# Optimization experiments

Measured on AMD Instinct MI355X. Metric: run time of the kernel, lower is better.

## Reference

```python
import jax, jax.numpy as jnp
import numpy as np

# Mamba2 defaults with d_model=512, headdim=2*d_model (=> nheads=1)
D_MODEL = 512
D_INNER = 2 * D_MODEL          # expand=2
D_STATE = 128
NHEADS = 1                     # d_inner // headdim = 1
HEADDIM = D_INNER              # headdim = 2*hidden_dim
D_CONV = 4
NG = 1                         # ngroups
EPS = 1e-5


def setup_inputs() -> dict:
    key = jax.random.key(0)
    ks = jax.random.split(key, 8)
    B, L = 4, 2048
    d_in_proj = 2 * D_INNER + 2 * NG * D_STATE + NHEADS   # 2305
    conv_ch = D_INNER + 2 * NG * D_STATE                  # 1280
    x = jax.random.normal(ks[0], (B, L, D_MODEL), jnp.float32)
    rnn_state = jax.random.normal(ks[1], (B, D_MODEL), jnp.float32)
    W_in = jax.random.normal(ks[2], (d_in_proj, D_MODEL), jnp.float32) * (D_MODEL ** -0.5)
    conv_w = jax.random.normal(ks[3], (conv_ch, 1, D_CONV), jnp.float32) * (D_CONV ** -0.5)
    conv_b = jnp.zeros((conv_ch,), jnp.float32)
    # dt_bias = inv_softplus(dt) with dt ~ U(1e-3, 0.1), as in Mamba2 init
    dt = jax.random.uniform(ks[4], (NHEADS,), jnp.float32, 1e-3, 0.1)
    dt_bias = jnp.log(jnp.expm1(dt))
    A_log = jnp.log(jax.random.uniform(ks[5], (NHEADS,), jnp.float32, 1.0, 16.0))
    Dp = jnp.ones((NHEADS,), jnp.float32)
    norm_w = jnp.ones((D_INNER,), jnp.float32)
    W_out = jax.random.normal(ks[6], (D_MODEL, D_INNER), jnp.float32) * (D_INNER ** -0.5)
    return dict(x=x, rnn_state=rnn_state, W_in=W_in, conv_w=conv_w, conv_b=conv_b,
                dt_bias=dt_bias, A_log=A_log, Dp=Dp, norm_w=norm_w, W_out=W_out)


def _mamba2(x, W_in, conv_w, conv_b, dt_bias, A_log, Dp, norm_w, W_out):
    B, L, _ = x.shape
    zxbcdt = jnp.einsum('bld,ed->ble', x, W_in)           # (B,L,2305)
    z, xBC, dt = jnp.split(zxbcdt, [D_INNER, 2 * D_INNER + 2 * NG * D_STATE], axis=-1)
    # causal depthwise conv1d over channels (B,C,L), then silu
    xBC = xBC.transpose(0, 2, 1)
    xBC = jax.lax.conv_general_dilated(
        xBC, conv_w, window_strides=(1,), padding=[(D_CONV - 1, 0)],
        feature_group_count=xBC.shape[1], dimension_numbers=('NCH', 'OIH', 'NCH'))
    xBC = jax.nn.silu(xBC + conv_b[None, :, None]).transpose(0, 2, 1)
    xs, Bm, Cm = jnp.split(xBC, [D_INNER, D_INNER + NG * D_STATE], axis=-1)
    xs = xs.reshape(B, L, NHEADS, HEADDIM)
    dt = jax.nn.softplus(dt + dt_bias)                    # (B,L,H)
    A = -jnp.exp(A_log)                                   # (H,)
    dA = jnp.exp(dt * A)                                  # (B,L,H)

    # selective state-space scan: h_t = dA_t*h_{t-1} + dt_t * x_t (x) B_t ; y_t = h_t @ C_t
    def step(state, inp):
        x_t, dt_t, dA_t, B_t, C_t = inp
        state = dA_t[:, :, None, None] * state \
            + (dt_t[:, :, None] * x_t)[..., None] * B_t[:, None, None, :]
        y_t = jnp.einsum('bhpn,bn->bhp', state, C_t)
        return state, y_t

    init = jnp.zeros((B, NHEADS, HEADDIM, D_STATE), x.dtype)
    inputs = (xs.transpose(1, 0, 2, 3), dt.transpose(1, 0, 2), dA.transpose(1, 0, 2),
              Bm.transpose(1, 0, 2), Cm.transpose(1, 0, 2))
    _, ys = jax.lax.scan(step, init, inputs)              # (L,B,H,P)
    y = ys.transpose(1, 0, 2, 3) + Dp[None, None, :, None] * xs
    y = y.reshape(B, L, D_INNER)
    # gated RMSNorm (gate first, norm_before_gate=False)
    y = y * jax.nn.silu(z)
    y = y * jax.lax.rsqrt(jnp.mean(y * y, axis=-1, keepdims=True) + EPS) * norm_w
    return jnp.einsum('bld,od->blo', y, W_out)


def reference(x, rnn_state, W_in, conv_w, conv_b, dt_bias, A_log, Dp, norm_w, W_out):
    out = _mamba2(x, W_in, conv_w, conv_b, dt_bias, A_log, Dp, norm_w, W_out)
    return (out, rnn_state)
```

## Files before the change

kernel.cpp:

```cpp
#include <hip/hip_runtime.h>
#include <cstdint>
#include <cstddef>


typedef __bf16 bf16_t;
typedef __bf16 bf16x8 __attribute__((ext_vector_type(8)));
typedef __bf16 bf16x4 __attribute__((ext_vector_type(4)));
typedef __bf16 bf16x2 __attribute__((ext_vector_type(2)));
typedef float  f32x4  __attribute__((ext_vector_type(4)));

#define BATCH   4
#define SEQLEN  2048
#define MROWS   8192
#define DMODEL  512
#define DINNER  1024
#define DSTATE  128
#define NZX     2304
#define NCONV   1280
#define CHUNK   128
#define NCHUNK  16
#define NBC     64

__device__ __forceinline__ float siluf(float x) { return x / (1.f + __expf(-x)); }

__device__ __forceinline__ void load_lds16(const bf16_t* g, bf16_t* l)
{
    __builtin_amdgcn_global_load_lds(
        (const __attribute__((address_space(1))) void*)g,
        (__attribute__((address_space(3))) void*)l,
        16, 0, 0);
}

template <typename OutT>
__device__ __forceinline__ void gemm64_body(
    unsigned char* smem,
    const bf16_t* __restrict__ A, const bf16_t* __restrict__ B,
    OutT* __restrict__ C, int Ntot, int K, int lda, int ldb, int bn, int bm)
{
    bf16_t* As = (bf16_t*)smem;
    bf16_t* Bs = (bf16_t*)(smem + 8192);

    const int tid  = threadIdx.x;
    const int wave = tid >> 6, lane = tid & 63;
    const int lr = lane & 15, q = lane >> 4;
    const int wm = (wave & 1) * 32, wn = (wave >> 1) * 64;

    f32x4 acc[2][4];
    #pragma unroll
    for (int i = 0; i < 2; ++i)
        #pragma unroll
        for (int j = 0; j < 4; ++j)
            acc[i][j] = (f32x4){0.f, 0.f, 0.f, 0.f};

    const int row_a0 = bm * 64, row_b0 = bn * 128;
    const int srow = tid >> 3;
    const int gsw  = (((tid & 7) ^ (srow & 7))) * 8;
    const int lsl  = (tid & 7) * 8;

    for (int kt = 0; kt < K; kt += 64) {
        #pragma unroll
        for (int i = 0; i < 2; ++i) {
            int row = srow + i * 32;
            load_lds16(&A[(size_t)(row_a0 + row) * lda + kt + gsw], &As[row * 64 + lsl]);
        }
        #pragma unroll
        for (int i = 0; i < 4; ++i) {
            int row = srow + i * 32;
            load_lds16(&B[(size_t)(row_b0 + row) * ldb + kt + gsw], &Bs[row * 64 + lsl]);
        }
        __syncthreads();
        #pragma unroll
        for (int k0 = 0; k0 < 64; k0 += 32) {
            bf16x8 af[2], bfr[4];
            #pragma unroll
            for (int mi = 0; mi < 2; ++mi) {
                int r = wm + mi * 16 + lr, kc = (k0 >> 3) + q;
                af[mi] = *reinterpret_cast<const bf16x8*>(
                    &As[r * 64 + ((kc ^ (r & 7)) << 3)]);
            }
            #pragma unroll
            for (int ni = 0; ni < 4; ++ni) {
                int r = wn + ni * 16 + lr, kc = (k0 >> 3) + q;
                bfr[ni] = *reinterpret_cast<const bf16x8*>(
                    &Bs[r * 64 + ((kc ^ (r & 7)) << 3)]);
            }
            #pragma unroll
            for (int mi = 0; mi < 2; ++mi)
                #pragma unroll
                for (int ni = 0; ni < 4; ++ni)
                    acc[mi][ni] = __builtin_amdgcn_mfma_f32_16x16x32_bf16(
                        af[mi], bfr[ni], acc[mi][ni], 0, 0, 0);
        }
        __syncthreads();
    }

    #pragma unroll
    for (int mi = 0; mi < 2; ++mi)
        #pragma unroll
        for (int ni = 0; ni < 4; ++ni)
            #pragma unroll
            for (int ri = 0; ri < 4; ++ri) {
                int row = row_a0 + wm + mi * 16 + q * 4 + ri;
                int col = row_b0 + wn + ni * 16 + lr;
                C[(size_t)row * Ntot + col] = (OutT)acc[mi][ni][ri];
            }
}

template <typename OutT>
__device__ __forceinline__ void gemm6464_body(
    unsigned char* smem,
    const bf16_t* __restrict__ A, const bf16_t* __restrict__ B,
    OutT* __restrict__ C, int Ntot, int K, int lda, int ldb, int bn, int bm)
{
    bf16_t* As = (bf16_t*)smem;
    bf16_t* Bs = (bf16_t*)(smem + 8192);

    const int tid  = threadIdx.x;
    const int wave = tid >> 6, lane = tid & 63;
    const int lr = lane & 15, q = lane >> 4;
    const int wm = (wave & 1) * 32, wn = (wave >> 1) * 32;

    f32x4 acc[2][2];
    #pragma unroll
    for (int i = 0; i < 2; ++i)
        #pragma unroll
        for (int j = 0; j < 2; ++j)
            acc[i][j] = (f32x4){0.f, 0.f, 0.f, 0.f};

    const int row_a0 = bm * 64, row_b0 = bn * 64;
    const int srow = tid >> 3;
    const int gsw  = (((tid & 7) ^ (srow & 7))) * 8;
    const int lsl  = (tid & 7) * 8;

    for (int kt = 0; kt < K; kt += 64) {
        #pragma unroll
        for (int i = 0; i < 2; ++i) {
            int row = srow + i * 32;
            load_lds16(&A[(size_t)(row_a0 + row) * lda + kt + gsw], &As[row * 64 + lsl]);
            load_lds16(&B[(size_t)(row_b0 + row) * ldb + kt + gsw], &Bs[row * 64 + lsl]);
        }
        __syncthreads();
        #pragma unroll
        for (int k0 = 0; k0 < 64; k0 += 32) {
            bf16x8 af[2], bfr[2];
            #pragma unroll
            for (int mi = 0; mi < 2; ++mi) {
                int r = wm + mi * 16 + lr, kc = (k0 >> 3) + q;
                af[mi] = *reinterpret_cast<const bf16x8*>(
                    &As[r * 64 + ((kc ^ (r & 7)) << 3)]);
            }
            #pragma unroll
            for (int ni = 0; ni < 2; ++ni) {
                int r = wn + ni * 16 + lr, kc = (k0 >> 3) + q;
                bfr[ni] = *reinterpret_cast<const bf16x8*>(
                    &Bs[r * 64 + ((kc ^ (r & 7)) << 3)]);
            }
            #pragma unroll
            for (int mi = 0; mi < 2; ++mi)
                #pragma unroll
                for (int ni = 0; ni < 2; ++ni)
                    acc[mi][ni] = __builtin_amdgcn_mfma_f32_16x16x32_bf16(
                        af[mi], bfr[ni], acc[mi][ni], 0, 0, 0);
        }
        __syncthreads();
    }

    #pragma unroll
    for (int mi = 0; mi < 2; ++mi)
        #pragma unroll
        for (int ni = 0; ni < 2; ++ni)
            #pragma unroll
            for (int ri = 0; ri < 4; ++ri) {
                int row = row_a0 + wm + mi * 16 + q * 4 + ri;
                int col = row_b0 + wn + ni * 16 + lr;
                C[(size_t)row * Ntot + col] = (OutT)acc[mi][ni][ri];
            }
}

__device__ __forceinline__ void cumsum_body(
    const float* __restrict__ dtv, const float* __restrict__ A_log,
    float* __restrict__ sarr, float* __restrict__ Pv,
    float* __restrict__ EdTv, float* __restrict__ chp, int bc)
{
    __shared__ float w0sum, stot;
    int j = threadIdx.x;
    bool active = j < CHUNK;
    int lane = j & 63;
    int r = bc * CHUNK + j;
    float A = -expf(A_log[0]);
    float dt = active ? dtv[r] : 0.f;
    float s = dt;
    #pragma unroll
    for (int m = 1; m <= 32; m <<= 1) {
        float o = __shfl_up(s, m);
        if (lane >= m) s += o;
    }
    if (j == 63) w0sum = s;
    __syncthreads();
    if (j >= 64 && active) s += w0sum;
    if (j == 127) stot = s;
    __syncthreads();
    if (active) {
        float sT = stot;
        sarr[r] = s;
        Pv[r]   = expf(A * s);
        EdTv[r] = expf(A * (sT - s)) * dt;
        if (j == 127) chp[bc] = expf(A * sT);
    }
}

__global__ __launch_bounds__(256) void gemm1_kernel(
    const bf16_t* __restrict__ xb, const bf16_t* __restrict__ winb,
    bf16_t* __restrict__ zx, const float* __restrict__ dtv,
    const float* __restrict__ A_log, float* __restrict__ sarr,
    float* __restrict__ Pv, float* __restrict__ EdTv, float* __restrict__ chp)
{
    __shared__ __align__(16) unsigned char smem[24576];
    int linear = blockIdx.x;
    if (linear < (NZX / 128) * (MROWS / 64)) {
        int xcd = linear & 7, j = linear >> 3;
        int bm = xcd * 16 + (j & 15);
        int bn = j >> 4;
        gemm64_body<bf16_t>(smem, xb, winb, zx, NZX, DMODEL, DMODEL, DMODEL, bn, bm);
    } else {
        cumsum_body(dtv, A_log, sarr, Pv, EdTv, chp, linear - 2304);
    }
}

__global__ __launch_bounds__(256) void gemm2_kernel(
    const bf16_t* __restrict__ yb, const bf16_t* __restrict__ woutb,
    float* __restrict__ out)
{
    __shared__ __align__(16) unsigned char smem[16384];
    int id  = blockIdx.x;
    int xcd = id & 7, j = id >> 3;
    int bm  = xcd * 16 + (j & 15);
    int bn  = j >> 4;
    gemm6464_body<float>(smem, yb, woutb, out, DMODEL, DINNER, DINNER, DINNER, bn, bm);
}

__global__ __launch_bounds__(256) void gemmA_kernel(
    const bf16_t* __restrict__ Xt, const bf16_t* __restrict__ Bwt,
    bf16_t* __restrict__ cstate)
{
    __shared__ __align__(16) unsigned char smem[16384];
    int id = blockIdx.x;
    int bc = id & 63;
    int t  = id >> 6;
    int bm = t >> 1, bn = t & 1;
    gemm6464_body<bf16_t>(smem,
        Xt + (size_t)bc * 131072, Bwt + (size_t)bc * 16384,
        cstate + (size_t)bc * 131072,
        DSTATE, CHUNK, CHUNK, CHUNK, bn, bm);
}

__device__ __forceinline__ void mbuild64_body(
    unsigned char* smem,
    const float* __restrict__ sarr, const float* __restrict__ dtv,
    const float* __restrict__ Pv, const float* __restrict__ A_log,
    const bf16_t* __restrict__ xbc, bf16_t* __restrict__ Mx, int sub)
{
    int bc = sub & 63;
    int t  = sub >> 6;
    int bm = t >> 1, bn = t & 1;

    bf16_t* Cs  = (bf16_t*)smem;
    bf16_t* Bs2 = (bf16_t*)(smem + 16384);
    float* sj = (float*)(smem + 32768);
    float* dj = sj + 128;
    float* pj = dj + 128;

    int tid = threadIdx.x;
    if (tid < CHUNK) {
        sj[tid] = sarr[bc * CHUNK + tid];
        dj[tid] = dtv[bc * CHUNK + tid];
        pj[tid] = Pv[bc * CHUNK + tid];
    }
    int rowbase = bc * 128;
    int srow = tid >> 4;
    int gsw  = (((tid & 15) ^ (srow & 7))) * 8;
    int lsl  = (tid & 15) * 8;
    #pragma unroll
    for (int i = 0; i < 4; ++i) {
        int row = srow + i * 16;
        load_lds16(&xbc[(size_t)(rowbase + bm * 64 + row) * NCONV + 1152 + gsw],
                   &Cs[row * 128 + lsl]);
        load_lds16(&xbc[(size_t)(rowbase + bn * 64 + row) * NCONV + 1024 + gsw],
                   &Bs2[row * 128 + lsl]);
    }
    __syncthreads();

    const int wave = tid >> 6, lane = tid & 63;
    const int lr = lane & 15, q = lane >> 4;
    const int wm = (wave & 1) * 32, wn = (wave >> 1) * 32;

    f32x4 acc[2][2];
    #pragma unroll
    for (int i = 0; i < 2; ++i)
        #pragma unroll
        for (int j = 0; j < 2; ++j)
            acc[i][j] = (f32x4){0.f, 0.f, 0.f, 0.f};

    #pragma unroll
    for (int k0 = 0; k0 < 128; k0 += 32) {
        bf16x8 af[2], bfr[2];
        #pragma unroll
        for (int mi = 0; mi < 2; ++mi) {
            int r = wm + mi * 16 + lr, kc = (k0 >> 3) + q;
            af[mi] = *reinterpret_cast<const bf16x8*>(
                &Cs[r * 128 + ((kc ^ (r & 7)) << 3)]);
        }
        #pragma unroll
        for (int ni = 0; ni < 2; ++ni) {
            int r = wn + ni * 16 + lr, kc = (k0 >> 3) + q;
            bfr[ni] = *reinterpret_cast<const bf16x8*>(
                &Bs2[r * 128 + ((kc ^ (r & 7)) << 3)]);
        }
        #pragma unroll
        for (int mi = 0; mi < 2; ++mi)
            #pragma unroll
            for (int ni = 0; ni < 2; ++ni)
                acc[mi][ni] = __builtin_amdgcn_mfma_f32_16x16x32_bf16(
                    af[mi], bfr[ni], acc[mi][ni], 0, 0, 0);
    }

    float A = -expf(A_log[0]);
    bf16_t* MxB = Mx + (size_t)bc * 32768;
    #pragma unroll
    for (int mi = 0; mi < 2; ++mi)
        #pragma unroll
        for (int ni = 0; ni < 2; ++ni)
            #pragma unroll
            for (int ri = 0; ri < 4; ++ri) {
                int row = bm * 64 + wm + mi * 16 + q * 4 + ri;
                int col = bn * 64 + wn + ni * 16 + lr;
                float val = 0.f;
                if (col <= row)
                    val = acc[mi][ni][ri] * expf(A * (sj[row] - sj[col])) * dj[col];
                MxB[(size_t)row * 256 + col] = (bf16_t)val;
            }

    if (bn == 0) {
        int rl = tid >> 2;
        int cb2 = (tid & 3) * 32;
        float Pi = pj[bm * 64 + rl];
        #pragma unroll
        for (int m0 = 0; m0 < 32; m0 += 8) {
            int kc = (cb2 + m0) >> 3;
            bf16x8 cv = *reinterpret_cast<const bf16x8*>(
                &Cs[rl * 128 + ((kc ^ (rl & 7)) << 3)]);
            bf16x8 o;
            #pragma unroll
            for (int m = 0; m < 8; ++m) o[m] = (bf16_t)((float)cv[m] * Pi);
            *reinterpret_cast<bf16x8*>(
                &MxB[(size_t)(bm * 64 + rl) * 256 + 128 + cb2 + m0]) = o;
        }
    }
}

__device__ __forceinline__ void scan_body(
    unsigned char* smem,
    const bf16_t* __restrict__ cstate, const float* __restrict__ chp,
    bf16_t* __restrict__ Stb, int blk)
{
    float* chS = (float*)smem;
    int idx = blk * 256 + threadIdx.x;
    int b   = idx >> 17;
    int np  = idx & 131071;
    if (threadIdx.x < NCHUNK) chS[threadIdx.x] = chp[b * NCHUNK + threadIdx.x];
    __syncthreads();

    const bf16_t* src = cstate + ((size_t)b << 21) + np;
    bf16_t*       dst = Stb    + ((size_t)b << 21) + np;
    float t[NCHUNK];
    #pragma unroll
    for (int c = 0; c < NCHUNK; ++c) t[c] = (float)src[(size_t)c << 17];
    float v = 0.f;
    #pragma unroll
    for (int c = 0; c < NCHUNK; ++c) {
        dst[(size_t)c << 17] = (bf16_t)v;
        v = chS[c] * v + t[c];
    }
}

__global__ __launch_bounds__(256) void scan_mbuild_kernel(
    const bf16_t* __restrict__ cstate, const float* __restrict__ chp,
    bf16_t* __restrict__ Stb,
    const float* __restrict__ sarr, const float* __restrict__ dtv,
    const float* __restrict__ Pv, const float* __restrict__ A_log,
    const bf16_t* __restrict__ xbc, bf16_t* __restrict__ Mx)
{
    __shared__ __align__(16) unsigned char smem[34304];
    int id = blockIdx.x;
    if (id < 256) {
        mbuild64_body(smem, sarr, dtv, Pv, A_log, xbc, Mx, id);
    } else {
        scan_body(smem, cstate, chp, Stb, id - 256);
    }
}

__global__ __launch_bounds__(256) void gemm_y_kernel(
    const bf16_t* __restrict__ Mx, const bf16_t* __restrict__ Xt,
    const bf16_t* __restrict__ Stb, bf16_t* __restrict__ yf)
{
    __shared__ __align__(16) bf16_t As[64 * 64];
    __shared__ __align__(16) bf16_t Bs[64 * 64];

    int id = blockIdx.x;
    int bc = id & 63;
    int t  = id >> 6;
    int half = t & 1, bn = t >> 1;

    const bf16_t* Ab = Mx  + (size_t)bc * 32768 + (size_t)half * 64 * 256;
    const bf16_t* Xb = Xt  + (size_t)bc * 131072 + (size_t)bn * 64 * 128;
    const bf16_t* Sb = Stb + (size_t)bc * 131072 + (size_t)bn * 64 * 128;
    bf16_t* Cb = yf + (size_t)bc * 131072 + (size_t)half * 64 * 1024;

    const int tid  = threadIdx.x;
    const int wave = tid >> 6, lane = tid & 63;
    const int lr = lane & 15, q = lane >> 4;
    const int wm = (wave & 1) * 32, wn = (wave >> 1) * 32;

    f32x4 acc[2][2];
    #pragma unroll
    for (int i = 0; i < 2; ++i)
        #pragma unroll
        for (int j = 0; j < 2; ++j)
            acc[i][j] = (f32x4){0.f, 0.f, 0.f, 0.f};

    const int srow = tid >> 3;
    const int gsw  = (((tid & 7) ^ (srow & 7))) * 8;
    const int lsl  = (tid & 7) * 8;

    for (int kt = 0; kt < 256; kt += 64) {
        const bf16_t* bsrc = (kt < 128) ? (Xb + kt) : (Sb + (kt - 128));
        #pragma unroll
        for (int i = 0; i < 2; ++i) {
            int row = srow + i * 32;
            load_lds16(&Ab[(size_t)row * 256 + kt + gsw], &As[row * 64 + lsl]);
            load_lds16(&bsrc[(size_t)row * 128 + gsw], &Bs[row * 64 + lsl]);
        }
        __syncthreads();
        #pragma unroll
        for (int k0 = 0; k0 < 64; k0 += 32) {
            bf16x8 af[2], bfr[2];
            #pragma unroll
            for (int mi = 0; mi < 2; ++mi) {
                int r = wm + mi * 16 + lr, kc = (k0 >> 3) + q;
                af[mi] = *reinterpret_cast<const bf16x8*>(
                    &As[r * 64 + ((kc ^ (r & 7)) << 3)]);
            }
            #pragma unroll
            for (int ni = 0; ni < 2; ++ni) {
                int r = wn + ni * 16 + lr, kc = (k0 >> 3) + q;
                bfr[ni] = *reinterpret_cast<const bf16x8*>(
                    &Bs[r * 64 + ((kc ^ (r & 7)) << 3)]);
            }
            #pragma unroll
            for (int mi = 0; mi < 2; ++mi)
                #pragma unroll
                for (int ni = 0; ni < 2; ++ni)
                    acc[mi][ni] = __builtin_amdgcn_mfma_f32_16x16x32_bf16(
                        af[mi], bfr[ni], acc[mi][ni], 0, 0, 0);
        }
        __syncthreads();
    }

    #pragma unroll
    for (int mi = 0; mi < 2; ++mi)
        #pragma unroll
        for (int ni = 0; ni < 2; ++ni)
            #pragma unroll
            for (int ri = 0; ri < 4; ++ri) {
                int row = wm + mi * 16 + q * 4 + ri;
                int col = bn * 64 + wn + ni * 16 + lr;
                Cb[(size_t)row * 1024 + col] = (bf16_t)acc[mi][ni][ri];
            }
}

__global__ __launch_bounds__(256) void dtcast_kernel(
    const float* __restrict__ x, const float* __restrict__ W_in,
    const float* __restrict__ dt_bias, const float* __restrict__ W_out,
    float* __restrict__ dtv, bf16_t* __restrict__ xb,
    bf16_t* __restrict__ winb, bf16_t* __restrict__ woutb)
{
    int bid = blockIdx.x;
    if (bid < MROWS / 4) {
        int wave = threadIdx.x >> 6, lane = threadIdx.x & 63;
        int r = bid * 4 + wave;
        const float* xr = x + (size_t)r * DMODEL + lane * 8;
        const float* wr = W_in + (size_t)NZX * DMODEL + lane * 8;
        float4 a0 = *reinterpret_cast<const float4*>(xr);
        float4 a1 = *reinterpret_cast<const float4*>(xr + 4);
        float4 b0 = *reinterpret_cast<const float4*>(wr);
        float4 b1 = *reinterpret_cast<const float4*>(wr + 4);

        bf16x8 xo;
        xo[0] = (bf16_t)a0.x; xo[1] = (bf16_t)a0.y; xo[2] = (bf16_t)a0.z; xo[3] = (bf16_t)a0.w;
        xo[4] = (bf16_t)a1.x; xo[5] = (bf16_t)a1.y; xo[6] = (bf16_t)a1.z; xo[7] = (bf16_t)a1.w;
        *reinterpret_cast<bf16x8*>(xb + (size_t)r * DMODEL + lane * 8) = xo;

        float s = a0.x * b0.x + a0.y * b0.y + a0.z * b0.z + a0.w * b0.w
                + a1.x * b1.x + a1.y * b1.y + a1.z * b1.z + a1.w * b1.w;
        #pragma unroll
        for (int m = 32; m >= 1; m >>= 1) s += __shfl_xor(s, m);
        if (lane == 0) {
            float t  = s + dt_bias[0];
            dtv[r] = (t > 20.f) ? t : log1pf(expf(t));
        }
        return;
    }
    int i = (bid - MROWS / 4) * 256 + threadIdx.x;
    const int n4a = 2305 * DMODEL / 4, n4b = DMODEL * DINNER / 4;
    const float* src; bf16_t* dst; int j;
    if (i < n4a)            { src = W_in;  dst = winb;  j = i; }
    else if (i < n4a + n4b) { src = W_out; dst = woutb; j = i - n4a; }
    else return;
    float4 v = reinterpret_cast<const float4*>(src)[j];
    bf16x4 o;
    o[0] = (bf16_t)v.x; o[1] = (bf16_t)v.y; o[2] = (bf16_t)v.z; o[3] = (bf16_t)v.w;
    reinterpret_cast<bf16x4*>(dst)[j] = o;
}

__global__ __launch_bounds__(256) void conv_tr_kernel(
    const bf16_t* __restrict__ zx, const float* __restrict__ cw,
    const float* __restrict__ cb, const float* __restrict__ EdTv,
    bf16_t* __restrict__ xbc, bf16_t* __restrict__ Xt, bf16_t* __restrict__ Bwt)
{
    constexpr int TS = 66;
    __shared__ bf16_t tile[128 * TS];
    __shared__ float cwS[64 * 4];
    __shared__ float cbS[64];

    int id  = blockIdx.x;
    int xcd = id & 7;
    int k   = id >> 3;
    int bc  = xcd * 8 + (k & 7);
    int rest = k >> 3;
    int cg   = rest >> 1;
    int half = rest & 1;
    int c0   = cg * 128 + half * 64;
    int tid  = threadIdx.x;

    if (tid < 64) {
        float4 w = *reinterpret_cast<const float4*>(cw + (size_t)(c0 + tid) * 4);
        *reinterpret_cast<float4*>(&cwS[tid * 4]) = w;
        cbS[tid] = cb[c0 + tid];
    }
    __syncthreads();

    int lrow = tid >> 3;
    int lc8  = (tid & 7) * 8;
    int g0 = bc * 128;

    #pragma unroll
    for (int pass = 0; pass < 4; ++pass) {
        int row = pass * 32 + lrow;
        int g = g0 + row;
        int l = g & (SEQLEN - 1);
        float acc[8];
        #pragma unroll
        for (int m = 0; m < 8; ++m) acc[m] = cbS[lc8 + m];
        #pragma unroll
        for (int kk = 0; kk < 4; ++kk) {
            if (l + kk >= 3) {
                bf16x8 v = *reinterpret_cast<const bf16x8*>(
                    zx + (size_t)(g + kk - 3) * NZX + DINNER + c0 + lc8);
                #pragma unroll
                for (int m = 0; m < 8; ++m)
                    acc[m] += cwS[(lc8 + m) * 4 + kk] * (float)v[m];
            }
        }
        bf16x8 o;
        #pragma unroll
        for (int m = 0; m < 8; ++m) o[m] = (bf16_t)siluf(acc[m]);
        *reinterpret_cast<bf16x8*>(xbc + (size_t)g * NCONV + c0 + lc8) = o;
        if (cg < 9) {
            #pragma unroll
            for (int jj = 0; jj < 4; ++jj) {
                bf16x2 p; p[0] = o[jj * 2]; p[1] = o[jj * 2 + 1];
                *reinterpret_cast<bf16x2*>(&tile[row * TS + lc8 + jj * 2]) = p;
            }
        }
    }
    if (cg == 9) return;
    __syncthreads();

    const bool isB = (cg == 8);
    int jo = (tid >> 4) * 8;
    int i  = tid & 15;
    float sc[8];
    #pragma unroll
    for (int m = 0; m < 8; ++m)
        sc[m] = isB ? EdTv[bc * 128 + jo + m] : 1.f;

    #pragma unroll
    for (int pass = 0; pass < 4; ++pass) {
        int oc = pass * 16 + i;
        bf16x8 o;
        #pragma unroll
        for (int m = 0; m < 8; ++m)
            o[m] = (bf16_t)((float)tile[(jo + m) * TS + oc] * sc[m]);
        bf16_t* dst = isB
            ? (Bwt + (size_t)bc * 16384 + (size_t)(c0 - 1024 + oc) * 128 + jo)
            : (Xt + (size_t)bc * 131072 + (size_t)(c0 + oc) * 128 + jo);
        *reinterpret_cast<bf16x8*>(dst) = o;
    }
}

__global__ __launch_bounds__(256) void gate_norm_kernel(
    const bf16_t* __restrict__ yf, const bf16_t* __restrict__ zx,
    const bf16_t* __restrict__ xbc, const float* __restrict__ Dp,
    const float* __restrict__ norm_w, bf16_t* __restrict__ yb,
    const float* __restrict__ rnn, float* __restrict__ outTail)
{
    int blk = blockIdx.x, tid = threadIdx.x;
    if (blk >= MROWS / 4) {
        int i = (blk - MROWS / 4) * 256 + tid;
        if (i < BATCH * DMODEL) outTail[i] = rnn[i];
        return;
    }
    int wave = tid >> 6, lane = tid & 63;
    int r = blk * 4 + wave;
    int p0 = lane * 8, p1 = 512 + lane * 8;
    float D0 = Dp[0];

    bf16x8 y0 = *reinterpret_cast<const bf16x8*>(yf + (size_t)r * DINNER + p0);
    bf16x8 y1 = *reinterpret_cast<const bf16x8*>(yf + (size_t)r * DINNER + p1);
    bf16x8 z0 = *reinterpret_cast<const bf16x8*>(zx + (size_t)r * NZX + p0);
    bf16x8 z1 = *reinterpret_cast<const bf16x8*>(zx + (size_t)r * NZX + p1);
    bf16x8 x0 = *reinterpret_cast<const bf16x8*>(xbc + (size_t)r * NCONV + p0);
    bf16x8 x1 = *reinterpret_cast<const bf16x8*>(xbc + (size_t)r * NCONV + p1);

    float g[16];
    #pragma unroll
    for (int m = 0; m < 8; ++m) {
        g[m]     = ((float)y0[m] + D0 * (float)x0[m]) * siluf((float)z0[m]);
        g[8 + m] = ((float)y1[m] + D0 * (float)x1[m]) * siluf((float)z1[m]);
    }
    float ss = 0.f;
    #pragma unroll
    for (int m = 0; m < 16; ++m) ss += g[m] * g[m];
    #pragma unroll
    for (int m = 32; m >= 1; m >>= 1) ss += __shfl_xor(ss, m);
    float scale = rsqrtf(ss * (1.f / 1024.f) + 1e-5f);

    const float* nw = norm_w;
    float4 w0a = *reinterpret_cast<const float4*>(nw + p0);
    float4 w0b = *reinterpret_cast<const float4*>(nw + p0 + 4);
    float4 w1a = *reinterpret_cast<const float4*>(nw + p1);
    float4 w1b = *reinterpret_cast<const float4*>(nw + p1 + 4);
    float w[16] = {w0a.x, w0a.y, w0a.z, w0a.w, w0b.x, w0b.y, w0b.z, w0b.w,
                   w1a.x, w1a.y, w1a.z, w1a.w, w1b.x, w1b.y, w1b.z, w1b.w};
    bf16x8 o0, o1;
    #pragma unroll
    for (int m = 0; m < 8; ++m) {
        o0[m] = (bf16_t)(g[m] * scale * w[m]);
        o1[m] = (bf16_t)(g[8 + m] * scale * w[8 + m]);
    }
    *reinterpret_cast<bf16x8*>(yb + (size_t)r * DINNER + p0) = o0;
    *reinterpret_cast<bf16x8*>(yb + (size_t)r * DINNER + p1) = o1;
}

extern "C" void kernel_launch(void* const* d_in, const int* in_sizes, int n_in,
                              void* d_out, int out_size, void* d_ws, size_t ws_size,
                              hipStream_t stream)
{
    const float* x        = (const float*)d_in[0];
    const float* rnn      = (const float*)d_in[1];
    const float* W_in     = (const float*)d_in[2];
    const float* conv_w   = (const float*)d_in[3];
    const float* conv_b   = (const float*)d_in[4];
    const float* dt_bias  = (const float*)d_in[5];
    const float* A_log    = (const float*)d_in[6];
    const float* Dp       = (const float*)d_in[7];
    const float* norm_w   = (const float*)d_in[8];
    const float* W_out    = (const float*)d_in[9];
    float* out = (float*)d_out;

    char* ws = (char*)d_ws;
    bf16_t* xb     = (bf16_t*)(ws + 0);
    bf16_t* Mx     = (bf16_t*)(ws + 4194304);
    bf16_t* winb   = (bf16_t*)(ws + 8388608);
    bf16_t* woutb  = (bf16_t*)(ws + 10748928);
    bf16_t* zx     = (bf16_t*)(ws + 11797504);
    float*  dtv    = (float*) (ws + 49546240);
    float*  sarr   = (float*) (ws + 49579008);
    float*  Pv     = (float*) (ws + 49611776);
    float*  EdTv   = (float*) (ws + 49644544);
    float*  chp    = (float*) (ws + 49677312);
    bf16_t* xbcb   = (bf16_t*)(ws + 49677568);
    bf16_t* Xt     = (bf16_t*)(ws + 70649088);
    bf16_t* Bwt    = (bf16_t*)(ws + 87426304);
    bf16_t* cstate = (bf16_t*)(ws + 89523456);
    bf16_t* yf     = (bf16_t*)(ws + 89523456);
    bf16_t* Stb    = (bf16_t*)(ws + 106300672);
    bf16_t* yb     = (bf16_t*)(ws + 123077888);

    {
        const int n4a = 2305 * DMODEL / 4, n4b = DMODEL * DINNER / 4;
        int grid = MROWS / 4 + (n4a + n4b + 255) / 256;
        dtcast_kernel<<<grid, 256, 0, stream>>>(
            x, W_in, dt_bias, W_out, dtv, xb, winb, woutb);
    }

    gemm1_kernel<<<2304 + NBC, 256, 0, stream>>>(
        xb, winb, zx, dtv, A_log, sarr, Pv, EdTv, chp);

    conv_tr_kernel<<<1280, 256, 0, stream>>>(
        zx, conv_w, conv_b, EdTv, xbcb, Xt, Bwt);

    gemmA_kernel<<<2048, 256, 0, stream>>>(Xt, Bwt, cstate);

    scan_mbuild_kernel<<<256 + BATCH * 131072 / 256, 256, 0, stream>>>(
        cstate, chp, Stb, sarr, dtv, Pv, A_log, xbcb, Mx);

    gemm_y_kernel<<<2048, 256, 0, stream>>>(Mx, Xt, Stb, yf);

    gate_norm_kernel<<<MROWS / 4 + 8, 256, 0, stream>>>(
        yf, zx, xbcb, Dp, norm_w, yb, rnn, out + (size_t)MROWS * DMODEL);

    gemm2_kernel<<<1024, 256, 0, stream>>>(yb, woutb, out);
}
```

Before: 190.2 us.

## Fuse gating and RMSNorm into gemm_y epilogue and gemm2 row scaling

Removes the separate gate_norm kernel. gemm_y now applies the D skip and SiLU gate in its epilogue, writes the gated y in bf16, and accumulates per-row sum of squares with atomics into a buffer that the scan kernel zeroes. gemm2 applies the rsqrt row scale to its output, and norm_w is folded into W_out during the bf16 cast. This saves one launch plus a full read and write of the intermediate y, at the cost of atomics and an epilogue that stages results through LDS.

```diff
diff --git a/kernel.cpp b/kernel.cpp
--- a/kernel.cpp
+++ b/kernel.cpp
@@ -229,14 +229,85 @@
 
 __global__ __launch_bounds__(256) void gemm2_kernel(
     const bf16_t* __restrict__ yb, const bf16_t* __restrict__ woutb,
-    float* __restrict__ out)
-{
-    __shared__ __align__(16) unsigned char smem[16384];
+    const float* __restrict__ ss, float* __restrict__ out)
+{
+    __shared__ __align__(16) bf16_t As[64 * 64];
+    __shared__ __align__(16) bf16_t Bs[64 * 64];
+
     int id  = blockIdx.x;
     int xcd = id & 7, j = id >> 3;
     int bm  = xcd * 16 + (j & 15);
     int bn  = j >> 4;
-    gemm6464_body<float>(smem, yb, woutb, out, DMODEL, DINNER, DINNER, DINNER, bn, bm);
+
+    const int tid  = threadIdx.x;
+    const int wave = tid >> 6, lane = tid & 63;
+    const int lr = lane & 15, q = lane >> 4;
+    const int wm = (wave & 1) * 32, wn = (wave >> 1) * 32;
+
+    f32x4 acc[2][2];
+    #pragma unroll
+    for (int i = 0; i < 2; ++i)
+        #pragma unroll
+        for (int jj = 0; jj < 2; ++jj)
+            acc[i][jj] = (f32x4){0.f, 0.f, 0.f, 0.f};
+
+    const int row_a0 = bm * 64, row_b0 = bn * 64;
+    const int srow = tid >> 3;
+    const int gsw  = (((tid & 7) ^ (srow & 7))) * 8;
+    const int lsl  = (tid & 7) * 8;
+
+    for (int kt = 0; kt < DINNER; kt += 64) {
+        #pragma unroll
+        for (int i = 0; i < 2; ++i) {
+            int row = srow + i * 32;
+            load_lds16(&yb[(size_t)(row_a0 + row) * DINNER + kt + gsw], &As[row * 64 + lsl]);
+            load_lds16(&woutb[(size_t)(row_b0 + row) * DINNER + kt + gsw], &Bs[row * 64 + lsl]);
+        }
+        __syncthreads();
+        #pragma unroll
+        for (int k0 = 0; k0 < 64; k0 += 32) {
+            bf16x8 af[2], bfr[2];
+            #pragma unroll
+            for (int mi = 0; mi < 2; ++mi) {
+                int r = wm + mi * 16 + lr, kc = (k0 >> 3) + q;
+                af[mi] = *reinterpret_cast<const bf16x8*>(
+                    &As[r * 64 + ((kc ^ (r & 7)) << 3)]);
+            }
+            #pragma unroll
+            for (int ni = 0; ni < 2; ++ni) {
+                int r = wn + ni * 16 + lr, kc = (k0 >> 3) + q;
+                bfr[ni] = *reinterpret_cast<const bf16x8*>(
+                    &Bs[r * 64 + ((kc ^ (r & 7)) << 3)]);
+            }
+            #pragma unroll
+            for (int mi = 0; mi < 2; ++mi)
+                #pragma unroll
+                for (int ni = 0; ni < 2; ++ni)
+                    acc[mi][ni] = __builtin_amdgcn_mfma_f32_16x16x32_bf16(
+                        af[mi], bfr[ni], acc[mi][ni], 0, 0, 0);
+        }
+        __syncthreads();
+    }
+
+    float sc[2][4];
+    #pragma unroll
+    for (int mi = 0; mi < 2; ++mi)
+        #pragma unroll
+        for (int ri = 0; ri < 4; ++ri) {
+            int row = row_a0 + wm + mi * 16 + q * 4 + ri;
+            sc[mi][ri] = rsqrtf(ss[row] * (1.f / 1024.f) + 1e-5f);
+        }
+
+    #pragma unroll
+    for (int mi = 0; mi < 2; ++mi)
+        #pragma unroll
+        for (int ni = 0; ni < 2; ++ni)
+            #pragma unroll
+            for (int ri = 0; ri < 4; ++ri) {
+                int row = row_a0 + wm + mi * 16 + q * 4 + ri;
+                int col = row_b0 + wn + ni * 16 + lr;
+                out[(size_t)row * DMODEL + col] = acc[mi][ni][ri] * sc[mi][ri];
+            }
 }
 
 __global__ __launch_bounds__(256) void gemmA_kernel(
@@ -388,20 +459,26 @@
     bf16_t* __restrict__ Stb,
     const float* __restrict__ sarr, const float* __restrict__ dtv,
     const float* __restrict__ Pv, const float* __restrict__ A_log,
-    const bf16_t* __restrict__ xbc, bf16_t* __restrict__ Mx)
+    const bf16_t* __restrict__ xbc, bf16_t* __restrict__ Mx,
+    float* __restrict__ ss)
 {
     __shared__ __align__(16) unsigned char smem[34304];
     int id = blockIdx.x;
     if (id < 256) {
         mbuild64_body(smem, sarr, dtv, Pv, A_log, xbc, Mx, id);
+    } else if (id < 256 + BATCH * 131072 / 256) {
+        scan_body(smem, cstate, chp, Stb, id - 256);
     } else {
-        scan_body(smem, cstate, chp, Stb, id - 256);
+        int i = (id - 256 - BATCH * 131072 / 256) * 256 + threadIdx.x;
+        ss[i] = 0.f;
     }
 }
 
 __global__ __launch_bounds__(256) void gemm_y_kernel(
     const bf16_t* __restrict__ Mx, const bf16_t* __restrict__ Xt,
-    const bf16_t* __restrict__ Stb, bf16_t* __restrict__ yf)
+    const bf16_t* __restrict__ Stb, const bf16_t* __restrict__ zx,
+    const bf16_t* __restrict__ xbc, const float* __restrict__ Dp,
+    bf16_t* __restrict__ yb, float* __restrict__ ss)
 {
     __shared__ __align__(16) bf16_t As[64 * 64];
     __shared__ __align__(16) bf16_t Bs[64 * 64];
@@ -414,7 +491,6 @@
     const bf16_t* Ab = Mx  + (size_t)bc * 32768 + (size_t)half * 64 * 256;
     const bf16_t* Xb = Xt  + (size_t)bc * 131072 + (size_t)bn * 64 * 128;
     const bf16_t* Sb = Stb + (size_t)bc * 131072 + (size_t)bn * 64 * 128;
-    bf16_t* Cb = yf + (size_t)bc * 131072 + (size_t)half * 64 * 1024;
 
     const int tid  = threadIdx.x;
     const int wave = tid >> 6, lane = tid & 63;
@@ -466,6 +542,7 @@
         __syncthreads();
     }
 
+    bf16_t* Yt = As;
     #pragma unroll
     for (int mi = 0; mi < 2; ++mi)
         #pragma unroll
@@ -473,16 +550,44 @@
             #pragma unroll
             for (int ri = 0; ri < 4; ++ri) {
                 int row = wm + mi * 16 + q * 4 + ri;
-                int col = bn * 64 + wn + ni * 16 + lr;
-                Cb[(size_t)row * 1024 + col] = (bf16_t)acc[mi][ni][ri];
-            }
+                int col = wn + ni * 16 + lr;
+                int u = (row * 8 + (col >> 3)) ^ (row & 7);
+                Yt[u * 8 + (col & 7)] = (bf16_t)acc[mi][ni][ri];
+            }
+    __syncthreads();
+
+    const int rr = tid >> 2, cq = tid & 3;
+    const size_t rg = (size_t)bc * 128 + half * 64 + rr;
+    const float D0 = Dp[0];
+    float part = 0.f;
+    #pragma unroll
+    for (int j = 0; j < 2; ++j) {
+        int u = (rr * 8 + cq * 2 + j) ^ (rr & 7);
+        bf16x8 yv = *reinterpret_cast<const bf16x8*>(&Yt[u * 8]);
+        int colg = bn * 64 + cq * 16 + j * 8;
+        bf16x8 zv = *reinterpret_cast<const bf16x8*>(zx  + rg * NZX   + colg);
+        bf16x8 xv = *reinterpret_cast<const bf16x8*>(xbc + rg * NCONV + colg);
+        bf16x8 o;
+        #pragma unroll
+        for (int m = 0; m < 8; ++m) {
+            float g = ((float)yv[m] + D0 * (float)xv[m]) * siluf((float)zv[m]);
+            part += g * g;
+            o[m] = (bf16_t)g;
+        }
+        *reinterpret_cast<bf16x8*>(yb + rg * DINNER + colg) = o;
+    }
+    part += __shfl_xor(part, 1);
+    part += __shfl_xor(part, 2);
+    if ((tid & 3) == 0) atomicAdd(&ss[rg], part);
 }
 
 __global__ __launch_bounds__(256) void dtcast_kernel(
     const float* __restrict__ x, const float* __restrict__ W_in,
     const float* __restrict__ dt_bias, const float* __restrict__ W_out,
+    const float* __restrict__ norm_w, const float* __restrict__ rnn,
     float* __restrict__ dtv, bf16_t* __restrict__ xb,
-    bf16_t* __restrict__ winb, bf16_t* __restrict__ woutb)
+    bf16_t* __restrict__ winb, bf16_t* __restrict__ woutb,
+    float* __restrict__ outTail)
 {
     int bid = blockIdx.x;
     if (bid < MROWS / 4) {
@@ -512,14 +617,24 @@
     }
     int i = (bid - MROWS / 4) * 256 + threadIdx.x;
     const int n4a = 2305 * DMODEL / 4, n4b = DMODEL * DINNER / 4;
-    const float* src; bf16_t* dst; int j;
-    if (i < n4a)            { src = W_in;  dst = winb;  j = i; }
-    else if (i < n4a + n4b) { src = W_out; dst = woutb; j = i - n4a; }
-    else return;
-    float4 v = reinterpret_cast<const float4*>(src)[j];
-    bf16x4 o;
-    o[0] = (bf16_t)v.x; o[1] = (bf16_t)v.y; o[2] = (bf16_t)v.z; o[3] = (bf16_t)v.w;
-    reinterpret_cast<bf16x4*>(dst)[j] = o;
+    if (i < n4a) {
+        float4 v = reinterpret_cast<const float4*>(W_in)[i];
+        bf16x4 o;
+        o[0] = (bf16_t)v.x; o[1] = (bf16_t)v.y; o[2] = (bf16_t)v.z; o[3] = (bf16_t)v.w;
+        reinterpret_cast<bf16x4*>(winb)[i] = o;
+    } else if (i < n4a + n4b) {
+        int j = i - n4a;
+        float4 v = reinterpret_cast<const float4*>(W_out)[j];
+        int c0 = (j * 4) & (DINNER - 1);
+        float4 w = *reinterpret_cast<const float4*>(norm_w + c0);
+        bf16x4 o;
+        o[0] = (bf16_t)(v.x * w.x); o[1] = (bf16_t)(v.y * w.y);
+        o[2] = (bf16_t)(v.z * w.z); o[3] = (bf16_t)(v.w * w.w);
+        reinterpret_cast<bf16x4*>(woutb)[j] = o;
+    } else if (i < n4a + n4b + BATCH * DMODEL) {
+        int k = i - n4a - n4b;
+        outTail[k] = rnn[k];
+    }
 }
 
 __global__ __launch_bounds__(256) void conv_tr_kernel(
@@ -606,60 +721,6 @@
             : (Xt + (size_t)bc * 131072 + (size_t)(c0 + oc) * 128 + jo);
         *reinterpret_cast<bf16x8*>(dst) = o;
     }
-}
-
-__global__ __launch_bounds__(256) void gate_norm_kernel(
-    const bf16_t* __restrict__ yf, const bf16_t* __restrict__ zx,
-    const bf16_t* __restrict__ xbc, const float* __restrict__ Dp,
-    const float* __restrict__ norm_w, bf16_t* __restrict__ yb,
-    const float* __restrict__ rnn, float* __restrict__ outTail)
-{
-    int blk = blockIdx.x, tid = threadIdx.x;
-    if (blk >= MROWS / 4) {
-        int i = (blk - MROWS / 4) * 256 + tid;
-        if (i < BATCH * DMODEL) outTail[i] = rnn[i];
-        return;
-    }
-    int wave = tid >> 6, lane = tid & 63;
-    int r = blk * 4 + wave;
-    int p0 = lane * 8, p1 = 512 + lane * 8;
-    float D0 = Dp[0];
-
-    bf16x8 y0 = *reinterpret_cast<const bf16x8*>(yf + (size_t)r * DINNER + p0);
-    bf16x8 y1 = *reinterpret_cast<const bf16x8*>(yf + (size_t)r * DINNER + p1);
-    bf16x8 z0 = *reinterpret_cast<const bf16x8*>(zx + (size_t)r * NZX + p0);
-    bf16x8 z1 = *reinterpret_cast<const bf16x8*>(zx + (size_t)r * NZX + p1);
-    bf16x8 x0 = *reinterpret_cast<const bf16x8*>(xbc + (size_t)r * NCONV + p0);
-    bf16x8 x1 = *reinterpret_cast<const bf16x8*>(xbc + (size_t)r * NCONV + p1);
-
-    float g[16];
-    #pragma unroll
-    for (int m = 0; m < 8; ++m) {
-        g[m]     = ((float)y0[m] + D0 * (float)x0[m]) * siluf((float)z0[m]);
-        g[8 + m] = ((float)y1[m] + D0 * (float)x1[m]) * siluf((float)z1[m]);
-    }
-    float ss = 0.f;
-    #pragma unroll
-    for (int m = 0; m < 16; ++m) ss += g[m] * g[m];
-    #pragma unroll
-    for (int m = 32; m >= 1; m >>= 1) ss += __shfl_xor(ss, m);
-    float scale = rsqrtf(ss * (1.f / 1024.f) + 1e-5f);
-
-    const float* nw = norm_w;
-    float4 w0a = *reinterpret_cast<const float4*>(nw + p0);
-    float4 w0b = *reinterpret_cast<const float4*>(nw + p0 + 4);
-    float4 w1a = *reinterpret_cast<const float4*>(nw + p1);
-    float4 w1b = *reinterpret_cast<const float4*>(nw + p1 + 4);
-    float w[16] = {w0a.x, w0a.y, w0a.z, w0a.w, w0b.x, w0b.y, w0b.z, w0b.w,
-                   w1a.x, w1a.y, w1a.z, w1a.w, w1b.x, w1b.y, w1b.z, w1b.w};
-    bf16x8 o0, o1;
-    #pragma unroll
-    for (int m = 0; m < 8; ++m) {
-        o0[m] = (bf16_t)(g[m] * scale * w[m]);
-        o1[m] = (bf16_t)(g[8 + m] * scale * w[8 + m]);
-    }
-    *reinterpret_cast<bf16x8*>(yb + (size_t)r * DINNER + p0) = o0;
-    *reinterpret_cast<bf16x8*>(yb + (size_t)r * DINNER + p1) = o1;
 }
 
 extern "C" void kernel_launch(void* const* d_in, const int* in_sizes, int n_in,
@@ -680,6 +741,7 @@
 
     char* ws = (char*)d_ws;
     bf16_t* xb     = (bf16_t*)(ws + 0);
+    float*  ssn    = (float*) (ws + 0);
     bf16_t* Mx     = (bf16_t*)(ws + 4194304);
     bf16_t* winb   = (bf16_t*)(ws + 8388608);
     bf16_t* woutb  = (bf16_t*)(ws + 10748928);
@@ -693,15 +755,16 @@
     bf16_t* Xt     = (bf16_t*)(ws + 70649088);
     bf16_t* Bwt    = (bf16_t*)(ws + 87426304);
     bf16_t* cstate = (bf16_t*)(ws + 89523456);
-    bf16_t* yf     = (bf16_t*)(ws + 89523456);
     bf16_t* Stb    = (bf16_t*)(ws + 106300672);
     bf16_t* yb     = (bf16_t*)(ws + 123077888);
 
     {
         const int n4a = 2305 * DMODEL / 4, n4b = DMODEL * DINNER / 4;
-        int grid = MROWS / 4 + (n4a + n4b + 255) / 256;
+        int nrest = n4a + n4b + BATCH * DMODEL;
+        int grid = MROWS / 4 + (nrest + 255) / 256;
         dtcast_kernel<<<grid, 256, 0, stream>>>(
-            x, W_in, dt_bias, W_out, dtv, xb, winb, woutb);
+            x, W_in, dt_bias, W_out, norm_w, rnn, dtv, xb, winb, woutb,
+            out + (size_t)MROWS * DMODEL);
     }
 
     gemm1_kernel<<<2304 + NBC, 256, 0, stream>>>(
@@ -712,13 +775,11 @@
 
     gemmA_kernel<<<2048, 256, 0, stream>>>(Xt, Bwt, cstate);
 
-    scan_mbuild_kernel<<<256 + BATCH * 131072 / 256, 256, 0, stream>>>(
-        cstate, chp, Stb, sarr, dtv, Pv, A_log, xbcb, Mx);
-
-    gemm_y_kernel<<<2048, 256, 0, stream>>>(Mx, Xt, Stb, yf);
-
-    gate_norm_kernel<<<MROWS / 4 + 8, 256, 0, stream>>>(
-        yf, zx, xbcb, Dp, norm_w, yb, rnn, out + (size_t)MROWS * DMODEL);
-
-    gemm2_kernel<<<1024, 256, 0, stream>>>(yb, woutb, out);
-}
+    scan_mbuild_kernel<<<256 + BATCH * 131072 / 256 + 32, 256, 0, stream>>>(
+        cstate, chp, Stb, sarr, dtv, Pv, A_log, xbcb, Mx, ssn);
+
+    gemm_y_kernel<<<2048, 256, 0, stream>>>(
+        Mx, Xt, Stb, zx, xbcb, Dp, yb, ssn);
+
+    gemm2_kernel<<<1024, 256, 0, stream>>>(yb, woutb, ssn, out);
+}
```

Measured after the change: 182.7 us, median of 2. -4.0%, faster.
